# Performance work log

Measured on AMD Instinct MI355X. Metric: run time of the kernel, lower is better.

## Reference

```python
import jax, jax.numpy as jnp
import numpy as np

EMB = 1024
HEADS = 16
HEAD_DIM = EMB // HEADS


def setup_inputs() -> dict:
    key = jax.random.key(0)
    ks = jax.random.split(key, 11)
    B, S = 2, 2048
    scale = 1.0 / np.sqrt(EMB)
    inp = {
        "query": jax.random.normal(ks[0], (B, S, EMB), jnp.float32),
        "key": jax.random.normal(ks[1], (B, S, EMB), jnp.float32),
        "value": jax.random.normal(ks[2], (B, S, EMB), jnp.float32),
        "Wq": jax.random.normal(ks[3], (EMB, EMB), jnp.float32) * scale,
        "bq": jnp.zeros((EMB,), jnp.float32),
        "Wk": jax.random.normal(ks[4], (EMB, EMB), jnp.float32) * scale,
        "bk": jnp.zeros((EMB,), jnp.float32),
        "Wv": jax.random.normal(ks[5], (EMB, EMB), jnp.float32) * scale,
        "bv": jnp.zeros((EMB,), jnp.float32),
        "Wo": jax.random.normal(ks[6], (EMB, EMB), jnp.float32) * scale,
        "bo": jnp.zeros((EMB,), jnp.float32),
    }
    return inp


def reference(query, key, value, Wq, bq, Wk, bk, Wv, bv, Wo, bo):
    B, S, _ = query.shape
    # Linear projections (torch Linear: x @ W.T + b)
    Q = query @ Wq.T + bq
    K = key @ Wk.T + bk
    V = value @ Wv.T + bv
    # [B, H, S, Dh]
    Q = Q.reshape(B, S, HEADS, HEAD_DIM).transpose(0, 2, 1, 3)
    K = K.reshape(B, S, HEADS, HEAD_DIM).transpose(0, 2, 1, 3)
    V = V.reshape(B, S, HEADS, HEAD_DIM).transpose(0, 2, 1, 3)
    scores = jnp.einsum("bhqd,bhkd->bhqk", Q, K) / jnp.sqrt(
        jnp.asarray(HEAD_DIM, Q.dtype)
    )
    attn = jax.nn.softmax(scores, axis=-1)
    ctx = jnp.einsum("bhqk,bhkd->bhqd", attn, V)
    ctx = ctx.transpose(0, 2, 1, 3).reshape(B, S, EMB)
    return ctx @ Wo.T + bo
```

## Files before the change

### kernel.cpp

```cpp
#include <hip/hip_runtime.h>
#include <stdint.h>

typedef __attribute__((ext_vector_type(8)))  __bf16 bf16x8;
typedef __attribute__((ext_vector_type(4)))  float  f32x4;
typedef __attribute__((ext_vector_type(16))) float  f32x16;
typedef __attribute__((ext_vector_type(8)))  ushort u16x8;
typedef __attribute__((ext_vector_type(4)))  ushort u16x4;
typedef __attribute__((ext_vector_type(4)))  uint   u32x4;

#define LOG2E 1.44269504088896f

__device__ __forceinline__ ushort f2bf(float f) {
  uint32_t u = __float_as_uint(f);
  u += 0x7fffu + ((u >> 16) & 1u);
  return (ushort)(u >> 16);
}
__device__ __forceinline__ float bf2f(ushort h) {
  return __uint_as_float(((uint32_t)h) << 16);
}
__device__ __forceinline__ void gload16(const void* g, void* l) {
  __builtin_amdgcn_global_load_lds((const __attribute__((address_space(1))) void*)g,
                                   (__attribute__((address_space(3))) void*)l, 16, 0, 0);
}
__device__ __forceinline__ f32x4 mfma16(bf16x8 a, bf16x8 b, f32x4 c) {
  return __builtin_amdgcn_mfma_f32_16x16x32_bf16(a, b, c, 0, 0, 0);
}
__device__ __forceinline__ f32x16 mfma32(bf16x8 a, bf16x8 b, f32x16 c) {
  return __builtin_amdgcn_mfma_f32_32x32x16_bf16(a, b, c, 0, 0, 0);
}
__device__ __forceinline__ int swz(int row, int byteoff) {
  return row * 128 + (byteoff ^ ((row & 7) << 4));
}
__device__ __forceinline__ uint cvtpk(float lo, float hi) {
  uint w;
  asm("v_cvt_pk_bf16_f32 %0, %1, %2" : "=v"(w) : "v"(lo), "v"(hi));
  return w;
}
__device__ __forceinline__ void plswap(uint& a, uint& b) {
  asm("v_permlane32_swap_b32 %0, %1" : "+v"(a), "+v"(b));
}

struct CvtArgs { const float* src[7]; ushort* dst[7]; };

__global__ __launch_bounds__(256) void cvt_all(CvtArgs a) {
  const int bid = blockIdx.x;
  int seg, base;
  if (bid < 2048) { seg = bid >> 9;              base = bid & 511; }
  else            { seg = 4 + ((bid - 2048) >> 11); base = (bid - 2048) & 2047; }
  const int i = base * 256 + threadIdx.x;
  const f32x4* s = (const f32x4*)a.src[seg];
  f32x4 x = s[2 * i], y = s[2 * i + 1];
  u16x8 o;
  o[0] = f2bf(x[0]); o[1] = f2bf(x[1]); o[2] = f2bf(x[2]); o[3] = f2bf(x[3]);
  o[4] = f2bf(y[0]); o[5] = f2bf(y[1]); o[6] = f2bf(y[2]); o[7] = f2bf(y[3]);
  ((u16x8*)a.dst[seg])[i] = o;
}

struct QKVArgs {
  const ushort* A0; const ushort* A1; const ushort* A2;
  const ushort* W0; const ushort* W1; const ushort* W2;
  const float* b0; const float* b1; const float* b2;
  ushort* Qo; ushort* Ko; ushort* Vo;
};

__global__ __launch_bounds__(256) void qkv_gemm(QKVArgs args) {
  __shared__ ushort Ash[2][128 * 64];
  __shared__ ushort Bsh[2][128 * 64];

  const int z = blockIdx.z;
  const ushort* Ab   = z == 0 ? args.A0 : (z == 1 ? args.A1 : args.A2);
  const ushort* Wb   = z == 0 ? args.W0 : (z == 1 ? args.W1 : args.W2);
  const float*  bias = z == 0 ? args.b0 : (z == 1 ? args.b1 : args.b2);

  const int tid = threadIdx.x;
  const int lane = tid & 63, wid = tid >> 6;
  const int l15 = lane & 15, g = lane >> 4;
  const int wr = wid >> 1, wc = wid & 1;
  const int tm = blockIdx.x * 128, tn = blockIdx.y * 128;

  const f32x4 fz = {0.f, 0.f, 0.f, 0.f};
  f32x4 acc[4][4];
#pragma unroll
  for (int m = 0; m < 4; ++m)
#pragma unroll
    for (int n = 0; n < 4; ++n) acc[m][n] = fz;

  const int srow8 = lane >> 3;
  const int ssl   = (lane & 7) ^ srow8;

#define QSTAGE(buf, kt)                                                       \
  {                                                                           \
    _Pragma("unroll")                                                         \
    for (int c = 0; c < 4; ++c) {                                             \
      const int chunk = wid * 4 + c;                                          \
      const int row = chunk * 8 + srow8;                                      \
      gload16(Wb + (size_t)(tn + row) * 1024 + (kt) + ssl * 8,                \
              &Bsh[buf][chunk * 512]);                                        \
      gload16(Ab + (size_t)(tm + row) * 1024 + (kt) + ssl * 8,                \
              &Ash[buf][chunk * 512]);                                        \
    }                                                                         \
  }

  QSTAGE(0, 0);
  __syncthreads();

  for (int kt = 0, t = 0; kt < 1024; kt += 64, ++t) {
    const int cur = t & 1;
    if (kt + 64 < 1024) QSTAGE(cur ^ 1, kt + 64);

#pragma unroll
    for (int kk = 0; kk < 2; ++kk) {
      bf16x8 af[4], bfr[4];
#pragma unroll
      for (int m = 0; m < 4; ++m) {
        const int row = wr * 64 + m * 16 + l15;
        af[m] = *(const bf16x8*)&Ash[cur][row * 64 + (((kk * 4 + g) ^ (row & 7)) * 8)];
      }
#pragma unroll
      for (int n = 0; n < 4; ++n) {
        const int row = wc * 64 + n * 16 + l15;
        bfr[n] = *(const bf16x8*)&Bsh[cur][row * 64 + (((kk * 4 + g) ^ (row & 7)) * 8)];
      }
#pragma unroll
      for (int m = 0; m < 4; ++m)
#pragma unroll
        for (int n = 0; n < 4; ++n) acc[m][n] = mfma16(af[m], bfr[n], acc[m][n]);
    }

    if (kt + 64 < 1024) __syncthreads();
  }
#undef QSTAGE

#pragma unroll
  for (int n = 0; n < 4; ++n) {
    const int col = tn + wc * 64 + n * 16 + l15;
    const float bv = bias[col];
    const int h = col >> 6, d = col & 63;
#pragma unroll
    for (int m = 0; m < 4; ++m) {
      const int row0 = tm + wr * 64 + m * 16 + g * 4;
      if (z == 2) {
        const int b = row0 >> 11, s0 = row0 & 2047;
        u16x4 pk;
#pragma unroll
        for (int r = 0; r < 4; ++r) pk[r] = f2bf(acc[m][n][r] + bv);
        *(u16x4*)&args.Vo[((size_t)((b * 16 + h) * 64 + d)) * 2048 + s0] = pk;
      } else {
        ushort* O = z ? args.Ko : args.Qo;
#pragma unroll
        for (int r = 0; r < 4; ++r) {
          const int row = row0 + r;
          const int b = row >> 11, s = row & 2047;
          O[((size_t)(b * 16 + h) * 2048 + s) * 64 + d] = f2bf(acc[m][n][r] + bv);
        }
      }
    }
  }
}

__global__ __launch_bounds__(256) void attn_fwd(const ushort* __restrict__ Qb,
                                                const ushort* __restrict__ Kb,
                                                const ushort* __restrict__ VTb,
                                                ushort* __restrict__ ctxb) {
  __shared__ char Ksh[64 * 128];
  __shared__ char Vsh[64 * 128];
  __shared__ float Ssc[4][32];

  const int tid = threadIdx.x;
  const int lane = tid & 63, wid = tid >> 6;
  const int l31 = lane & 31, hi = lane >> 5;
  const int bh = blockIdx.y;
  const int q0 = blockIdx.x * 128 + wid * 32;

  const ushort* Qh = Qb + (size_t)bh * 2048 * 64;
  const ushort* Kh = Kb + (size_t)bh * 2048 * 64;
  const ushort* Vh = VTb + (size_t)bh * 64 * 2048;

  bf16x8 qf[4];
  {
    const ushort* qrow = Qh + (size_t)(q0 + l31) * 64;
#pragma unroll
    for (int dt = 0; dt < 4; ++dt) {
      u16x8 raw = *(const u16x8*)&qrow[dt * 16 + hi * 8];
      u16x8 sc;
#pragma unroll
      for (int j = 0; j < 8; ++j) sc[j] = f2bf(bf2f(raw[j]) * 0.125f);
      qf[dt] = __builtin_bit_cast(bf16x8, sc);
    }
  }

  f32x16 o0 = {}, o1 = {};
  float m = -1e30f, lsum = 0.f;

  const int si = tid >> 2, sc4i = tid & 3;
  const ushort* kg = &Kh[(size_t)si * 64 + sc4i * 16];
  const ushort* vg = &Vh[(size_t)si * 2048 + sc4i * 16];

  u16x8 kr0, kr1, vr0, vr1;
  kr0 = *(const u16x8*)kg;  kr1 = *(const u16x8*)(kg + 8);
  vr0 = *(const u16x8*)vg;  vr1 = *(const u16x8*)(vg + 8);
  *(u16x8*)(Ksh + swz(si, sc4i * 32))      = kr0;
  *(u16x8*)(Ksh + swz(si, sc4i * 32 + 16)) = kr1;
  *(u16x8*)(Vsh + swz(si, sc4i * 32))      = vr0;
  *(u16x8*)(Vsh + swz(si, sc4i * 32 + 16)) = vr1;
  __syncthreads();

  for (int t = 0; t < 32; ++t) {
    if (t + 1 < 32) {
      const int kt2 = (t + 1) * 64;
      kr0 = *(const u16x8*)(kg + (size_t)kt2 * 64);
      kr1 = *(const u16x8*)(kg + (size_t)kt2 * 64 + 8);
      vr0 = *(const u16x8*)(vg + kt2);
      vr1 = *(const u16x8*)(vg + kt2 + 8);
    }

    f32x16 P0 = {}, P1 = {};
    __builtin_amdgcn_s_setprio(1);
#pragma unroll
    for (int dt = 0; dt < 4; ++dt) {
      bf16x8 kf0 = *(const bf16x8*)(Ksh + swz(l31,      dt * 32 + hi * 16));
      bf16x8 kf1 = *(const bf16x8*)(Ksh + swz(32 + l31, dt * 32 + hi * 16));
      P0 = mfma32(kf0, qf[dt], P0);
      P1 = mfma32(kf1, qf[dt], P1);
    }
    __builtin_amdgcn_s_setprio(0);

    float pm = fmaxf(P0[0], P1[0]);
#pragma unroll
    for (int r = 1; r + 1 < 16; r += 2) {
      pm = fmaxf(fmaxf(pm, P0[r]), P0[r + 1]);
      pm = fmaxf(fmaxf(pm, P1[r]), P1[r + 1]);
    }
    pm = fmaxf(fmaxf(pm, P0[15]), P1[15]);
    pm = fmaxf(pm, __shfl_xor(pm, 32));

    if (!__all(pm <= m + 8.f)) {
      const float mn = fmaxf(m, pm);
      const float scl = __builtin_amdgcn_exp2f((m - mn) * LOG2E);
      m = mn;
      lsum *= scl;
      Ssc[wid][l31] = scl;
      f32x4 s0 = *(const f32x4*)&Ssc[wid][hi * 4];
      f32x4 s1 = *(const f32x4*)&Ssc[wid][8 + hi * 4];
      f32x4 s2 = *(const f32x4*)&Ssc[wid][16 + hi * 4];
      f32x4 s3 = *(const f32x4*)&Ssc[wid][24 + hi * 4];
#pragma unroll
      for (int r = 0; r < 16; ++r) {
        const float sv = (r < 4 ? s0[r & 3] : r < 8 ? s1[r & 3] : r < 12 ? s2[r & 3] : s3[r & 3]);
        o0[r] *= sv; o1[r] *= sv;
      }
    }

    const float nml = -m * LOG2E;
#pragma unroll
    for (int r = 0; r < 16; ++r)
      P0[r] = __builtin_amdgcn_exp2f(__builtin_fmaf(P0[r], LOG2E, nml));
#pragma unroll
    for (int r = 0; r < 16; ++r)
      P1[r] = __builtin_amdgcn_exp2f(__builtin_fmaf(P1[r], LOG2E, nml));

    float rs = 0.f;
#pragma unroll
    for (int r = 0; r < 16; ++r) rs += P0[r] + P1[r];
    rs += __shfl_xor(rs, 32);
    lsum += rs;

    bf16x8 pa[4];
#pragma unroll
    for (int s = 0; s < 2; ++s) {
      const f32x16& P = s ? P1 : P0;
      uint a0 = cvtpk(P[0], P[1]),  b0 = cvtpk(P[4], P[5]);
      uint a1 = cvtpk(P[2], P[3]),  b1 = cvtpk(P[6], P[7]);
      plswap(a0, b0); plswap(a1, b1);
      pa[2 * s] = __builtin_bit_cast(bf16x8, (u32x4){a0, a1, b0, b1});
      uint a2 = cvtpk(P[8], P[9]),   b2 = cvtpk(P[12], P[13]);
      uint a3 = cvtpk(P[10], P[11]), b3 = cvtpk(P[14], P[15]);
      plswap(a2, b2); plswap(a3, b3);
      pa[2 * s + 1] = __builtin_bit_cast(bf16x8, (u32x4){a2, a3, b2, b3});
    }

    __builtin_amdgcn_s_setprio(1);
#pragma unroll
    for (int kk = 0; kk < 4; ++kk) {
      bf16x8 v0f = *(const bf16x8*)(Vsh + swz(l31,      kk * 32 + hi * 16));
      bf16x8 v1f = *(const bf16x8*)(Vsh + swz(32 + l31, kk * 32 + hi * 16));
      o0 = mfma32(pa[kk], v0f, o0);
      o1 = mfma32(pa[kk], v1f, o1);
    }
    __builtin_amdgcn_s_setprio(0);

    if (t + 1 < 32) {
      __syncthreads();
      *(u16x8*)(Ksh + swz(si, sc4i * 32))      = kr0;
      *(u16x8*)(Ksh + swz(si, sc4i * 32 + 16)) = kr1;
      *(u16x8*)(Vsh + swz(si, sc4i * 32))      = vr0;
      *(u16x8*)(Vsh + swz(si, sc4i * 32 + 16)) = vr1;
      __syncthreads();
    }
  }

  Ssc[wid][l31] = 1.0f / lsum;
  f32x4 i0 = *(const f32x4*)&Ssc[wid][hi * 4];
  f32x4 i1 = *(const f32x4*)&Ssc[wid][8 + hi * 4];
  f32x4 i2 = *(const f32x4*)&Ssc[wid][16 + hi * 4];
  f32x4 i3 = *(const f32x4*)&Ssc[wid][24 + hi * 4];
  const int b = bh >> 4, h = bh & 15;
#pragma unroll
  for (int r = 0; r < 16; ++r) {
    const float inv = (r < 4 ? i0[r & 3] : r < 8 ? i1[r & 3] : r < 12 ? i2[r & 3] : i3[r & 3]);
    const int q = q0 + (r & 3) + 8 * (r >> 2) + 4 * hi;
    const size_t base = ((size_t)(b * 2048 + q)) * 1024 + h * 64;
    ctxb[base + l31]      = f2bf(o0[r] * inv);
    ctxb[base + 32 + l31] = f2bf(o1[r] * inv);
  }
}

__global__ __launch_bounds__(256) void out_gemm(const ushort* __restrict__ A16,
                                                const ushort* __restrict__ Wb,
                                                const float* __restrict__ bias,
                                                float* __restrict__ O) {
  __shared__ ushort Ash[64 * 64];
  __shared__ ushort Bsh[128 * 64];

  const int tid = threadIdx.x;
  const int lane = tid & 63, wid = tid >> 6;
  const int l15 = lane & 15, g = lane >> 4;
  const int wr = wid >> 1, wc = wid & 1;
  const int tm = blockIdx.x * 64, tn = blockIdx.y * 128;

  const f32x4 fz = {0.f, 0.f, 0.f, 0.f};
  f32x4 acc[2][4];
#pragma unroll
  for (int m = 0; m < 2; ++m)
#pragma unroll
    for (int n = 0; n < 4; ++n) acc[m][n] = fz;

  const int srow8 = lane >> 3;
  const int ssl   = (lane & 7) ^ srow8;

  for (int kt = 0; kt < 1024; kt += 64) {
#pragma unroll
    for (int c = 0; c < 4; ++c) {
      const int chunk = wid * 4 + c;
      const int row = chunk * 8 + srow8;
      gload16(Wb + (size_t)(tn + row) * 1024 + kt + ssl * 8, &Bsh[chunk * 512]);
    }
#pragma unroll
    for (int c = 0; c < 2; ++c) {
      const int chunk = wid * 2 + c;
      const int row = chunk * 8 + srow8;
      gload16(A16 + (size_t)(tm + row) * 1024 + kt + ssl * 8, &Ash[chunk * 512]);
    }
    __syncthreads();

#pragma unroll
    for (int kk = 0; kk < 2; ++kk) {
      bf16x8 af[2], bfr[4];
#pragma unroll
      for (int m = 0; m < 2; ++m) {
        const int row = wr * 32 + m * 16 + l15;
        af[m] = *(const bf16x8*)&Ash[row * 64 + (((kk * 4 + g) ^ (row & 7)) * 8)];
      }
#pragma unroll
      for (int n = 0; n < 4; ++n) {
        const int row = wc * 64 + n * 16 + l15;
        bfr[n] = *(const bf16x8*)&Bsh[row * 64 + (((kk * 4 + g) ^ (row & 7)) * 8)];
      }
#pragma unroll
      for (int m = 0; m < 2; ++m)
#pragma unroll
        for (int n = 0; n < 4; ++n) acc[m][n] = mfma16(af[m], bfr[n], acc[m][n]);
    }
    __syncthreads();
  }

#pragma unroll
  for (int n = 0; n < 4; ++n) {
    const int col = tn + wc * 64 + n * 16 + l15;
    const float bv = bias[col];
#pragma unroll
    for (int m = 0; m < 2; ++m) {
      const int row0 = tm + wr * 32 + m * 16 + g * 4;
#pragma unroll
      for (int r = 0; r < 4; ++r)
        O[(size_t)(row0 + r) * 1024 + col] = acc[m][n][r] + bv;
    }
  }
}

extern "C" void kernel_launch(void* const* d_in, const int* in_sizes, int n_in,
                              void* d_out, int out_size, void* d_ws, size_t ws_size,
                              hipStream_t stream) {
  const float* query = (const float*)d_in[0];
  const float* key_  = (const float*)d_in[1];
  const float* value = (const float*)d_in[2];
  const float* Wq = (const float*)d_in[3];
  const float* bq = (const float*)d_in[4];
  const float* Wk = (const float*)d_in[5];
  const float* bk = (const float*)d_in[6];
  const float* Wv = (const float*)d_in[7];
  const float* bv = (const float*)d_in[8];
  const float* Wo = (const float*)d_in[9];
  const float* bo = (const float*)d_in[10];

  ushort* ws = (ushort*)d_ws;
  ushort* Wqb = ws;
  ushort* Wkb = ws + (1u << 20);
  ushort* Wvb = ws + (2u << 20);
  ushort* Wob = ws + (3u << 20);
  ushort* Qb  = ws + (4u << 20);
  ushort* Kb  = Qb + (4u << 20);
  ushort* VTb = Kb + (4u << 20);
  ushort* ctx = VTb + (4u << 20);
  ushort* Xqb = ctx;
  ushort* Xkb = (ushort*)d_out;
  ushort* Xvb = (ushort*)d_out + (4u << 20);

  dim3 blk(256);

  CvtArgs ca;
  ca.src[0] = Wq;    ca.dst[0] = Wqb;
  ca.src[1] = Wk;    ca.dst[1] = Wkb;
  ca.src[2] = Wv;    ca.dst[2] = Wvb;
  ca.src[3] = Wo;    ca.dst[3] = Wob;
  ca.src[4] = query; ca.dst[4] = Xqb;
  ca.src[5] = key_;  ca.dst[5] = Xkb;
  ca.src[6] = value; ca.dst[6] = Xvb;
  cvt_all<<<8192, blk, 0, stream>>>(ca);

  QKVArgs a;
  a.A0 = Xqb;  a.A1 = Xkb;  a.A2 = Xvb;
  a.W0 = Wqb;  a.W1 = Wkb;  a.W2 = Wvb;
  a.b0 = bq;   a.b1 = bk;   a.b2 = bv;
  a.Qo = Qb;   a.Ko = Kb;   a.Vo = VTb;
  qkv_gemm<<<dim3(32, 8, 3), blk, 0, stream>>>(a);

  attn_fwd<<<dim3(16, 32), blk, 0, stream>>>(Qb, Kb, VTb, ctx);

  out_gemm<<<dim3(64, 8), blk, 0, stream>>>(ctx, Wob, bo, (float*)d_out);
}
```

Measured before the change: 131.0 us.

## Triple-buffer QKV GEMM with BK=32 stages and explicit vmcnt waits

Restructures the QKV projection GEMM main loop from a double-buffered pipeline with 64-wide K tiles to a triple-buffered one with 32-wide K tiles. Loads are issued two stages ahead, and each step uses a partial s_waitcnt vmcnt instead of a full __syncthreads, so global-to-LDS loads stay in flight across iterations. The LDS swizzle is adapted to the narrower rows. The aim is more latency hiding with a smaller LDS footprint, at the cost of twice as many barriers and less MFMA work per stage. The hand-set vmcnt counts are fragile.

```diff
diff --git a/kernel.cpp b/kernel.cpp
--- a/kernel.cpp
+++ b/kernel.cpp
@@ -64,8 +64,8 @@
 };
 
 __global__ __launch_bounds__(256) void qkv_gemm(QKVArgs args) {
-  __shared__ ushort Ash[2][128 * 64];
-  __shared__ ushort Bsh[2][128 * 64];
+  __shared__ ushort Ash[3][128 * 32];
+  __shared__ ushort Bsh[3][128 * 32];
 
   const int z = blockIdx.z;
   const ushort* Ab   = z == 0 ? args.A0 : (z == 1 ? args.A1 : args.A2);
@@ -85,49 +85,56 @@
 #pragma unroll
     for (int n = 0; n < 4; ++n) acc[m][n] = fz;
 
-  const int srow8 = lane >> 3;
-  const int ssl   = (lane & 7) ^ srow8;
+  const int srow16 = lane >> 2;
+  const int ssl4   = (lane & 3) ^ ((srow16 >> 1) & 3);
 
 #define QSTAGE(buf, kt)                                                       \
   {                                                                           \
     _Pragma("unroll")                                                         \
-    for (int c = 0; c < 4; ++c) {                                             \
-      const int chunk = wid * 4 + c;                                          \
-      const int row = chunk * 8 + srow8;                                      \
-      gload16(Wb + (size_t)(tn + row) * 1024 + (kt) + ssl * 8,                \
+    for (int c = 0; c < 2; ++c) {                                             \
+      const int chunk = wid * 2 + c;                                          \
+      const int row = chunk * 16 + srow16;                                    \
+      gload16(Wb + (size_t)(tn + row) * 1024 + (kt) + ssl4 * 8,               \
               &Bsh[buf][chunk * 512]);                                        \
-      gload16(Ab + (size_t)(tm + row) * 1024 + (kt) + ssl * 8,                \
+      gload16(Ab + (size_t)(tm + row) * 1024 + (kt) + ssl4 * 8,               \
               &Ash[buf][chunk * 512]);                                        \
     }                                                                         \
   }
 
   QSTAGE(0, 0);
-  __syncthreads();
-
-  for (int kt = 0, t = 0; kt < 1024; kt += 64, ++t) {
-    const int cur = t & 1;
-    if (kt + 64 < 1024) QSTAGE(cur ^ 1, kt + 64);
-
-#pragma unroll
-    for (int kk = 0; kk < 2; ++kk) {
-      bf16x8 af[4], bfr[4];
-#pragma unroll
-      for (int m = 0; m < 4; ++m) {
-        const int row = wr * 64 + m * 16 + l15;
-        af[m] = *(const bf16x8*)&Ash[cur][row * 64 + (((kk * 4 + g) ^ (row & 7)) * 8)];
-      }
-#pragma unroll
-      for (int n = 0; n < 4; ++n) {
-        const int row = wc * 64 + n * 16 + l15;
-        bfr[n] = *(const bf16x8*)&Bsh[cur][row * 64 + (((kk * 4 + g) ^ (row & 7)) * 8)];
-      }
-#pragma unroll
-      for (int m = 0; m < 4; ++m)
-#pragma unroll
-        for (int n = 0; n < 4; ++n) acc[m][n] = mfma16(af[m], bfr[n], acc[m][n]);
-    }
-
-    if (kt + 64 < 1024) __syncthreads();
+  QSTAGE(1, 32);
+  asm volatile("s_waitcnt vmcnt(4)" ::: "memory");
+  __builtin_amdgcn_s_barrier();
+  __builtin_amdgcn_sched_barrier(0);
+
+#pragma unroll
+  for (int t = 0; t < 32; ++t) {
+    const int cur = t % 3;
+    const int kt = t * 32;
+    if (t + 2 < 32) QSTAGE((t + 2) % 3, kt + 64);
+
+    bf16x8 af[4], bfr[4];
+#pragma unroll
+    for (int m = 0; m < 4; ++m) {
+      const int row = wr * 64 + m * 16 + l15;
+      af[m] = *(const bf16x8*)&Ash[cur][row * 32 + ((g ^ ((row >> 1) & 3)) * 8)];
+    }
+#pragma unroll
+    for (int n = 0; n < 4; ++n) {
+      const int row = wc * 64 + n * 16 + l15;
+      bfr[n] = *(const bf16x8*)&Bsh[cur][row * 32 + ((g ^ ((row >> 1) & 3)) * 8)];
+    }
+#pragma unroll
+    for (int m = 0; m < 4; ++m)
+#pragma unroll
+      for (int n = 0; n < 4; ++n) acc[m][n] = mfma16(af[m], bfr[n], acc[m][n]);
+
+    if (t + 1 < 32) {
+      if (t + 2 < 32) asm volatile("s_waitcnt vmcnt(4)" ::: "memory");
+      else            asm volatile("s_waitcnt vmcnt(0)" ::: "memory");
+      __builtin_amdgcn_s_barrier();
+      __builtin_amdgcn_sched_barrier(0);
+    }
   }
 #undef QSTAGE
 
```

Measured after the change: 124.0 us, median of 2. 1.06x faster.
